# Kernel optimization log

Hardware: AMD Instinct MI355X
Metric: run time of the kernel (lower is better)

## Reference

```python
import jax, jax.numpy as jnp
import numpy as np

B, S, H, NH, DIS = 8, 512, 512, 8, 32
HD = H // NH  # head_dim = 64


def setup_inputs() -> dict:
    key = jax.random.key(0)
    ks = jax.random.split(key, 9)
    sc = 0.05
    return {
        "x": jax.random.normal(ks[0], (B, S, H), jnp.float32),
        "rel_distance": jax.random.randint(ks[1], (B, S, 2 * S), 0, DIS, jnp.int64),
        "mask": jnp.zeros((B, S, 2 * S), jnp.bool_),
        "query_pos_embedding": jax.random.normal(ks[2], (DIS, H), jnp.float32) * sc,
        "key_pos_embedding": jax.random.normal(ks[3], (DIS, H), jnp.float32) * sc,
        "value_pos_embedding": jax.random.normal(ks[4], (DIS, H), jnp.float32) * sc,
        "Wq": jax.random.normal(ks[5], (H, H), jnp.float32) * sc,
        "Wk": jax.random.normal(ks[6], (2 * H, H), jnp.float32) * sc,
        "Wv": jax.random.normal(ks[7], (2 * H, H), jnp.float32) * sc,
        "Wo": jax.random.normal(ks[8], (H, H), jnp.float32) * sc,
    }


def reference(x, rel_distance, mask, query_pos_embedding, key_pos_embedding,
              value_pos_embedding, Wq, Wk, Wv, Wo):
    b, s, _ = x.shape
    scale = jnp.sqrt(jnp.asarray(HD, x.dtype))

    # projections (torch Linear: y = x @ W.T)
    q = (x @ Wq.T).reshape(b, s, NH, HD).transpose(0, 2, 1, 3)        # [B,h,S,d]
    k = (x @ Wk.T).reshape(b, 2 * s, NH, HD).transpose(0, 2, 1, 3)    # [B,h,2S,d]
    v = (x @ Wv.T).reshape(b, 2 * s, NH, HD).transpose(0, 2, 1, 3)    # [B,h,2S,d]

    rel = jnp.broadcast_to(rel_distance[:, None], (b, NH, s, 2 * s))  # [B,h,S,2S]

    # relative-position weights via gather along distance axis
    q_emb = query_pos_embedding.reshape(DIS, NH, HD)                  # [n,h,d]
    qpw_full = jnp.einsum('bhsd,nhd->bhsn', q, q_emb)                 # [B,h,S,n]
    qpw = jnp.take_along_axis(qpw_full, rel, axis=3)                  # [B,h,S,2S]

    k_emb = key_pos_embedding.reshape(DIS, NH, HD)
    kpw_full = jnp.einsum('bhkd,nhd->bhkn', k, k_emb)                 # [B,h,2S,n]
    kpw = jnp.take_along_axis(kpw_full, rel.transpose(0, 1, 3, 2), axis=3)  # [B,h,2S,S]
    kpw = kpw.transpose(0, 1, 3, 2)                                   # [B,h,S,2S]

    scores = (jnp.einsum('bhsd,bhkd->bhsk', q, k) + qpw + kpw) / scale
    scores = jnp.where(mask[:, None], -jnp.inf, scores)
    probs = jax.nn.softmax(scores, axis=-1)                           # [B,h,S,2S]

    # scatter-add probs into distance buckets: [B,h,S,n]
    bi = jnp.arange(b)[:, None, None, None]
    hi = jnp.arange(NH)[None, :, None, None]
    si = jnp.arange(s)[None, None, :, None]
    vdw = jnp.zeros((b, NH, s, DIS), probs.dtype).at[bi, hi, si, rel].add(probs)

    v_emb = value_pos_embedding.reshape(DIS, NH, HD)                  # [n,h,d]
    out = jnp.einsum('bhsk,bhkd->bhsd', probs, v) \
        + jnp.einsum('bhsn,nhd->bhsd', vdw, v_emb)                    # [B,h,S,d]
    out = out.transpose(0, 2, 1, 3).reshape(b, s, H)
    return out @ Wo.T
```

## Files before the change

kernel.cpp:

```cpp
#include <hip/hip_runtime.h>
#include <math.h>

#define Bc 8
#define Sc 512
#define Hc 512
#define NHc 8
#define HDc 64
#define DISc 32
#define S2c 1024

typedef __attribute__((ext_vector_type(8))) short bf16x8;
typedef __attribute__((ext_vector_type(4))) float f32x4;
#define MFMA16(a, b, c) __builtin_amdgcn_mfma_f32_16x16x32_bf16(a, b, c, 0, 0, 0)

__device__ __forceinline__ unsigned short f2bf(float f) {
  unsigned u = __float_as_uint(f);
  return (unsigned short)((u + 0x7fffu + ((u >> 16) & 1u)) >> 16);
}
__device__ __forceinline__ float b2f(unsigned short u) {
  return __uint_as_float((unsigned)u << 16);
}
__device__ __forceinline__ bf16x8 ldb16x8(const unsigned short* p) {
  union { uint4 u; bf16x8 s; } cv;
  cv.u = *(const uint4*)p;
  return cv.s;
}
__device__ __forceinline__ void gll16(const unsigned short* g, void* l) {
  __builtin_amdgcn_global_load_lds(
      (const __attribute__((address_space(1))) unsigned int*)g,
      (__attribute__((address_space(3))) unsigned int*)l, 16, 0, 0);
}

__global__ __launch_bounds__(256) void cvt5_k(
    const float* __restrict__ x, const float* __restrict__ wq,
    const float* __restrict__ wk, const float* __restrict__ wv,
    const float* __restrict__ wo, unsigned short* __restrict__ x16,
    unsigned short* __restrict__ w16q, unsigned short* __restrict__ w16k,
    unsigned short* __restrict__ w16v, unsigned short* __restrict__ w16o) {
  int i = blockIdx.x * 256 + threadIdx.x;
  const float* src; unsigned short* dst; int off; float sc = 1.f;
  if (i < 524288)      { src = x;  dst = x16;  off = i; }
  else if (i < 589824) { src = wq; dst = w16q; off = i - 524288; sc = 0.125f; }
  else if (i < 720896) { src = wk; dst = w16k; off = i - 589824; }
  else if (i < 851968) { src = wv; dst = w16v; off = i - 720896; }
  else                 { src = wo; dst = w16o; off = i - 851968; }
  float4 v = ((const float4*)src)[off];
  ushort4 u;
  u.x = f2bf(v.x * sc); u.y = f2bf(v.y * sc);
  u.z = f2bf(v.z * sc); u.w = f2bf(v.w * sc);
  ((ushort4*)dst)[off] = u;
}

__global__ __launch_bounds__(256) void pack_k(const int* __restrict__ rel,
                                              const unsigned char* __restrict__ mask,
                                              unsigned char* __restrict__ pk8) {
  int i = blockIdx.x * 256 + threadIdx.x;
  const int* rp = rel + i * 16;
  uint4 mu = *(const uint4*)(mask + i * 16);
  const unsigned char* mb = (const unsigned char*)&mu;
  uint4 o;
  unsigned* ow = (unsigned*)&o;
#pragma unroll
  for (int g = 0; g < 4; ++g) {
    int4 r4 = ((const int4*)rp)[g];
    unsigned b0 = ((unsigned)r4.x & 31u) | (mb[g * 4 + 0] ? 0x80u : 0u);
    unsigned b1 = ((unsigned)r4.y & 31u) | (mb[g * 4 + 1] ? 0x80u : 0u);
    unsigned b2 = ((unsigned)r4.z & 31u) | (mb[g * 4 + 2] ? 0x80u : 0u);
    unsigned b3 = ((unsigned)r4.w & 31u) | (mb[g * 4 + 3] ? 0x80u : 0u);
    ow[g] = b0 | (b1 << 8) | (b2 << 16) | (b3 << 24);
  }
  *(uint4*)(pk8 + i * 16) = o;
}

__global__ __launch_bounds__(256) void wemb_k(
    const float* __restrict__ qpe, const float* __restrict__ kpe,
    const float* __restrict__ Wq, const float* __restrict__ Wk,
    unsigned short* __restrict__ wqp, unsigned short* __restrict__ wkp) {
  const int bid = blockIdx.x;
  const int cc = bid & 3, unit = bid >> 2;
  const int c0 = cc << 7;
  const int t = threadIdx.x;
  const float* emb; const float* Wsrc; unsigned short* outp; int rowbase, h;
  if (unit < 8) {
    h = unit; emb = qpe; Wsrc = Wq + (size_t)(h * 64) * 512; outp = wqp; rowbase = h * 32;
  } else {
    int u = unit - 8; int e = u >> 3; h = u & 7;
    emb = kpe; Wsrc = Wk + (size_t)(e * 512 + h * 64) * 512; outp = wkp;
    rowbase = e * 256 + h * 32;
  }
  __shared__ float es[32][65];
  __shared__ float wsh[64][132];
  {
    int n = t >> 3, d4 = (t & 7) << 3;
    float4 v0 = *(const float4*)(emb + (size_t)n * 512 + h * 64 + d4);
    float4 v1 = *(const float4*)(emb + (size_t)n * 512 + h * 64 + d4 + 4);
    *(float4*)&es[n][d4] = v0;
    *(float4*)&es[n][d4 + 4] = v1;
  }
#pragma unroll
  for (int p = 0; p < 8; ++p) {
    int slot = t + (p << 8);
    int d = slot >> 5, c4 = (slot & 31) << 2;
    *(float4*)&wsh[d][c4] = *(const float4*)(Wsrc + (size_t)d * 512 + c0 + c4);
  }
  __syncthreads();
  const int n = t >> 3, cb = (t & 7) << 4;
  float acc[16] = {};
#pragma unroll
  for (int d = 0; d < 64; ++d) {
    float ev = es[n][d];
    float4 w0 = *(const float4*)&wsh[d][cb];
    float4 w1 = *(const float4*)&wsh[d][cb + 4];
    float4 w2 = *(const float4*)&wsh[d][cb + 8];
    float4 w3 = *(const float4*)&wsh[d][cb + 12];
    acc[0] = fmaf(ev, w0.x, acc[0]);   acc[1] = fmaf(ev, w0.y, acc[1]);
    acc[2] = fmaf(ev, w0.z, acc[2]);   acc[3] = fmaf(ev, w0.w, acc[3]);
    acc[4] = fmaf(ev, w1.x, acc[4]);   acc[5] = fmaf(ev, w1.y, acc[5]);
    acc[6] = fmaf(ev, w1.z, acc[6]);   acc[7] = fmaf(ev, w1.w, acc[7]);
    acc[8] = fmaf(ev, w2.x, acc[8]);   acc[9] = fmaf(ev, w2.y, acc[9]);
    acc[10] = fmaf(ev, w2.z, acc[10]); acc[11] = fmaf(ev, w2.w, acc[11]);
    acc[12] = fmaf(ev, w3.x, acc[12]); acc[13] = fmaf(ev, w3.y, acc[13]);
    acc[14] = fmaf(ev, w3.z, acc[14]); acc[15] = fmaf(ev, w3.w, acc[15]);
  }
  unsigned short* orow = outp + (size_t)(rowbase + n) * 512 + c0 + cb;
#pragma unroll
  for (int j = 0; j < 16; ++j) orow[j] = f2bf(acc[j] * 0.125f);
}

template <int MODE>
__global__ __launch_bounds__(256, 4) void gemm16_k(
    const unsigned short* __restrict__ A, const unsigned short* __restrict__ B1,
    const unsigned short* __restrict__ B2, void* __restrict__ out1,
    void* __restrict__ out2, int M, int N, int K, int nsplit) {
  const int t = threadIdx.x;
  const int w = t >> 6, lane = t & 63, ln = lane & 15, qd = lane >> 4;
  const int wm = (w >> 1) << 6, wn = (w & 1) << 5;
  const int m0 = blockIdx.y << 7, n0 = blockIdx.x << 6;
  __shared__ __align__(16) unsigned short As[128 * 64];
  __shared__ __align__(16) unsigned short Bs[64 * 64];
  const bool reg1 = (n0 < nsplit);
  const unsigned short* Bb =
      reg1 ? B1 + (size_t)n0 * K : B2 + (size_t)(n0 - nsplit) * K;
  const int lr = lane >> 3, lc = (lane & 7) << 3;
  const unsigned short* ga = A + (size_t)(m0 + (w << 5) + lr) * K + lc;
  const unsigned short* gb = Bb + (size_t)((w << 4) + lr) * K + lc;
  char* lA = (char*)As + (w << 12);
  char* lB = (char*)Bs + (w << 11);
  f32x4 z = {0.f, 0.f, 0.f, 0.f};
  f32x4 acc[4][2] = {{z, z}, {z, z}, {z, z}, {z, z}};
  for (int k0 = 0; k0 < K; k0 += 64) {
#pragma unroll
    for (int i = 0; i < 4; ++i)
      gll16(ga + (size_t)(i << 3) * K + k0, lA + (i << 10));
#pragma unroll
    for (int i = 0; i < 2; ++i)
      gll16(gb + (size_t)(i << 3) * K + k0, lB + (i << 10));
    __syncthreads();
#pragma unroll
    for (int kk = 0; kk < 64; kk += 32) {
      bf16x8 af[4], bfr[2];
#pragma unroll
      for (int x = 0; x < 4; ++x)
        af[x] = ldb16x8(&As[(wm + x * 16 + ln) * 64 + kk + qd * 8]);
#pragma unroll
      for (int y = 0; y < 2; ++y)
        bfr[y] = ldb16x8(&Bs[(wn + y * 16 + ln) * 64 + kk + qd * 8]);
#pragma unroll
      for (int tm = 0; tm < 4; ++tm)
#pragma unroll
        for (int tn = 0; tn < 2; ++tn)
          acc[tm][tn] = MFMA16(af[tm], bfr[tn], acc[tm][tn]);
    }
    __syncthreads();
  }
#pragma unroll
  for (int tm = 0; tm < 4; ++tm)
#pragma unroll
    for (int tn = 0; tn < 2; ++tn)
#pragma unroll
      for (int r = 0; r < 4; ++r) {
        int m = m0 + wm + tm * 16 + qd * 4 + r;
        int n = n0 + wn + tn * 16 + ln;
        float v = acc[tm][tn][r];
        int bb = m >> 9, s = m & 511;
        if (MODE == 0) {
          ((float*)out1)[(size_t)m * N + n] = v;
        } else if (MODE == 3) {
          int e = n >> 9, hh = (n >> 6) & 7, d = n & 63;
          int k2 = 2 * s + e;
          ((unsigned short*)out1)[((size_t)(bb * 8 + hh) * 64 + d) * 1024 + k2] = f2bf(v);
        } else if (MODE == 1) {
          if (reg1) {
            int hh = (n >> 6) & 7, d = n & 63;
            ((unsigned short*)out1)[((size_t)(bb * 8 + hh) * 512 + s) * 64 + d] = f2bf(v);
          } else {
            int n2 = n - 512, hh = n2 >> 5, nn = n2 & 31;
            ((unsigned short*)out2)[((size_t)(bb * 8 + hh) * 512 + s) * 32 + nn] = f2bf(v);
          }
        } else {
          if (reg1) {
            int e = n >> 9, hh = (n >> 6) & 7, d = n & 63;
            int k2 = 2 * s + e;
            ((unsigned short*)out1)[((size_t)(bb * 8 + hh) * 1024 + k2) * 64 + d] = f2bf(v);
          } else {
            int n2 = n - 1024, e = n2 >> 8, hh = (n2 >> 5) & 7, nn = n2 & 31;
            int k2 = 2 * s + e;
            ((unsigned short*)out2)[((size_t)(bb * 8 + hh) * 1024 + k2) * 32 + nn] = f2bf(v);
          }
        }
      }
}

__global__ __launch_bounds__(512, 4) void attn6_k(
    const unsigned short* __restrict__ q16h, const unsigned short* __restrict__ kb16,
    const unsigned short* __restrict__ vT16, const unsigned short* __restrict__ qpw16,
    const unsigned short* __restrict__ kpw16, const unsigned char* __restrict__ pk8,
    const float* __restrict__ v_emb, unsigned short* __restrict__ attn16) {
  const int bid = blockIdx.x;
  const int b = bid & 7;
  const int h = (bid >> 3) & 7;
  const int qb = ((bid >> 6) & 7) << 6;
  const int t = threadIdx.x;
  const int w = t >> 6;
  const int g = w >> 2;
  const int ws4 = w & 3;
  const int lane = t & 63;
  const int ln = lane & 15;
  const int qd = lane >> 4;

  __shared__ __align__(16) char smem[60928];
  unsigned char*  pkt  = (unsigned char*)smem;
  unsigned short* kpws = (unsigned short*)(smem + 10240);
  unsigned short* q32s = (unsigned short*)(smem + 19456);
  unsigned short* pbuf = (unsigned short*)(smem + 24064);
  unsigned long long* vdwm64 = (unsigned long long*)(smem + 42496);
  float*          accbuf = (float*)smem;
  unsigned short* vest   = (unsigned short*)(smem + 24064);
  unsigned short* vdwb   = (unsigned short*)(smem + 29184);

  for (int i = t; i < 4 * 16 * 36; i += 512) vdwm64[i] = 0ull;
  if (t < 256) {
    int row = t >> 2, c8 = (t & 3) << 3;
    *(uint4*)&q32s[row * 36 + c8] =
        *(const uint4*)(qpw16 + ((size_t)((b * 8 + h) * 512 + qb) + row) * 32 + c8);
  }
  const unsigned short* kbase = kb16 + (size_t)(b * 8 + h) * 65536;
  const unsigned short* vbase = vT16 + (size_t)(b * 8 + h) * 65536;
  bf16x8 aQ[2];
  {
    const unsigned short* qsrc =
        q16h + ((size_t)((b * 8 + h) * 512 + qb + ws4 * 16 + ln)) * 64;
    aQ[0] = ldb16x8(qsrc + qd * 8);
    aQ[1] = ldb16x8(qsrc + 32 + qd * 8);
  }
  f32x4 z = {0.f, 0.f, 0.f, 0.f};
  f32x4 acc[4] = {z, z, z, z};

  const int u = t & 255, gg = t >> 8;
  const int qr = u >> 2, cg = (u & 3) << 4;
  const int kc8 = (u & 3) << 3;
  const unsigned char* pks = pk8 + ((size_t)(b * 512 + qb + qr)) * 1024 + (gg << 9);
  const unsigned short* kps =
      kpw16 + ((size_t)((b * 8 + h) * 1024) + (gg << 9) + qr) * 32 + kc8;
  unsigned char* pt_w = pkt + gg * 5120 + qr * 80 + cg;
  unsigned short* kp_w = kpws + gg * 2304 + qr * 36 + kc8;

  uint4 pv = *(const uint4*)(pks + cg);
  uint4 kv = *(const uint4*)kps;

  for (int kti = 0; kti < 8; ++kti) {
    *(uint4*)pt_w = pv;
    *(uint4*)kp_w = kv;
    __syncthreads();
    if (kti < 7) {
      pv = *(const uint4*)(pks + ((kti + 1) << 6) + cg);
      kv = *(const uint4*)(kps + ((size_t)(kti + 1) << 11));
    }
    const int kt0 = (kti + g * 8) << 6;

    f32x4 sc4[4];
#pragma unroll
    for (int t4 = 0; t4 < 4; ++t4) {
      f32x4 c = z;
      c = MFMA16(aQ[0], ldb16x8(kbase + (size_t)(kt0 + t4 * 16 + ln) * 64 + qd * 8), c);
      c = MFMA16(aQ[1], ldb16x8(kbase + (size_t)(kt0 + t4 * 16 + ln) * 64 + 32 + qd * 8), c);
      sc4[t4] = c;
    }

    unsigned char* pt_ = pkt + g * 5120;
    unsigned short* kp_ = kpws + g * 2304;
#pragma unroll
    for (int r = 0; r < 4; ++r) {
#pragma unroll
      for (int t4 = 0; t4 < 4; ++t4) {
        int row_l = ws4 * 16 + qd * 4 + r;
        int kl = t4 * 16 + ln;
        unsigned um = pt_[row_l * 80 + kl];
        int rd = um & 31;
        float s = sc4[t4][r] + b2f(q32s[row_l * 36 + rd]) + b2f(kp_[kl * 36 + rd]);
        float p = (um & 0x80u) ? 0.f : __expf(s);
        atomicAdd(&vdwm64[ws4 * 576 + (qd * 4 + r) * 36 + rd],
                  (unsigned long long)(p * 67108864.0f));
        pbuf[w * 1152 + (qd * 4 + r) * 72 + kl] = f2bf(p);
      }
    }

    bf16x8 a0 = ldb16x8(&pbuf[w * 1152 + ln * 72 + qd * 8]);
    bf16x8 a1 = ldb16x8(&pbuf[w * 1152 + ln * 72 + 32 + qd * 8]);
#pragma unroll
    for (int dt = 0; dt < 4; ++dt) {
      acc[dt] = MFMA16(a0, ldb16x8(vbase + (size_t)(dt * 16 + ln) * 1024 + kt0 + qd * 8), acc[dt]);
      acc[dt] = MFMA16(a1, ldb16x8(vbase + (size_t)(dt * 16 + ln) * 1024 + kt0 + 32 + qd * 8), acc[dt]);
    }
    __syncthreads();
  }

  if (t < 256) {
    int n = t >> 3, d0 = (t & 7) << 3;
    const float* src = v_emb + ((size_t)n << 9) + (h << 6) + d0;
    float4 f0 = *(const float4*)src;
    float4 f1 = *(const float4*)(src + 4);
    vest[(d0 + 0) * 40 + n] = f2bf(f0.x); vest[(d0 + 1) * 40 + n] = f2bf(f0.y);
    vest[(d0 + 2) * 40 + n] = f2bf(f0.z); vest[(d0 + 3) * 40 + n] = f2bf(f0.w);
    vest[(d0 + 4) * 40 + n] = f2bf(f1.x); vest[(d0 + 5) * 40 + n] = f2bf(f1.y);
    vest[(d0 + 6) * 40 + n] = f2bf(f1.z); vest[(d0 + 7) * 40 + n] = f2bf(f1.w);
  } else {
    int row = lane >> 2, n0 = (lane & 3) << 3;
    float vv[8];
#pragma unroll
    for (int j = 0; j < 8; ++j)
      vv[j] = (float)vdwm64[ws4 * 576 + row * 36 + n0 + j] * 1.4901161193847656e-8f;
    ushort4 u0, u1;
    u0.x = f2bf(vv[0]); u0.y = f2bf(vv[1]); u0.z = f2bf(vv[2]); u0.w = f2bf(vv[3]);
    u1.x = f2bf(vv[4]); u1.y = f2bf(vv[5]); u1.z = f2bf(vv[6]); u1.w = f2bf(vv[7]);
    *(ushort4*)&vdwb[ws4 * 640 + row * 40 + n0] = u0;
    *(ushort4*)&vdwb[ws4 * 640 + row * 40 + n0 + 4] = u1;
  }
  __syncthreads();

  if (g == 1) {
    bf16x8 av = ldb16x8(&vdwb[ws4 * 640 + ln * 40 + qd * 8]);
#pragma unroll
    for (int dt = 0; dt < 4; ++dt)
      acc[dt] = MFMA16(av, ldb16x8(&vest[(dt * 16 + ln) * 40 + qd * 8]), acc[dt]);
#pragma unroll
    for (int r = 0; r < 4; ++r)
#pragma unroll
      for (int dt = 0; dt < 4; ++dt)
        accbuf[ws4 * 1088 + (qd * 4 + r) * 68 + dt * 16 + ln] = acc[dt][r];
  }
  __syncthreads();

  if (g == 0) {
    float inv[4];
#pragma unroll
    for (int r = 0; r < 4; ++r) {
      unsigned long long lu = 0ull;
#pragma unroll
      for (int n = 0; n < 32; ++n)
        lu += vdwm64[ws4 * 576 + (qd * 4 + r) * 36 + n];
      inv[r] = 67108864.0f / (float)lu;
    }
    unsigned short* obase =
        attn16 + ((size_t)(b * 512 + qb + ws4 * 16 + qd * 4)) * 512 + (h << 6);
#pragma unroll
    for (int r = 0; r < 4; ++r)
#pragma unroll
      for (int dt = 0; dt < 4; ++dt) {
        float v = (acc[dt][r] + accbuf[ws4 * 1088 + (qd * 4 + r) * 68 + dt * 16 + ln]) * inv[r];
        obase[(size_t)r * 512 + dt * 16 + ln] = f2bf(v);
      }
  }
}

extern "C" void kernel_launch(void* const* d_in, const int* in_sizes, int n_in,
                              void* d_out, int out_size, void* d_ws, size_t ws_size,
                              hipStream_t stream) {
  const float* x = (const float*)d_in[0];
  const int* rel = (const int*)d_in[1];
  const unsigned char* mask = (const unsigned char*)d_in[2];
  const float* qpe = (const float*)d_in[3];
  const float* kpe = (const float*)d_in[4];
  const float* vpe = (const float*)d_in[5];
  const float* Wq = (const float*)d_in[6];
  const float* Wk = (const float*)d_in[7];
  const float* Wv = (const float*)d_in[8];
  const float* Wo = (const float*)d_in[9];
  float* out = (float*)d_out;

  unsigned short* u = (unsigned short*)d_ws;
  unsigned short* x16    = u;
  unsigned short* w16q   = x16 + 2097152;
  unsigned short* w16k   = w16q + 262144;
  unsigned short* w16v   = w16k + 524288;
  unsigned short* w16o   = w16v + 524288;
  unsigned short* wqp16  = w16o + 262144;
  unsigned short* wkp16  = wqp16 + 131072;
  unsigned short* q16h   = wkp16 + 262144;
  unsigned short* qpw16  = q16h + 2097152;
  unsigned short* kb16   = qpw16 + 1048576;
  unsigned short* kpw16  = kb16 + 4194304;
  unsigned short* vT16   = kpw16 + 2097152;
  unsigned short* attn16 = vT16 + 4194304;
  unsigned char* pk8 = (unsigned char*)(attn16 + 2097152);

  pack_k<<<1024, 256, 0, stream>>>(rel, mask, pk8);
  cvt5_k<<<3584, 256, 0, stream>>>(x, Wq, Wk, Wv, Wo, x16, w16q, w16k, w16v, w16o);
  wemb_k<<<96, 256, 0, stream>>>(qpe, kpe, Wq, Wk, wqp16, wkp16);
  gemm16_k<1><<<dim3(12, 32), 256, 0, stream>>>(x16, w16q, wqp16, q16h, qpw16,
                                                4096, 768, 512, 512);
  gemm16_k<2><<<dim3(24, 32), 256, 0, stream>>>(x16, w16k, wkp16, kb16, kpw16,
                                                4096, 1536, 512, 1024);
  gemm16_k<3><<<dim3(16, 32), 256, 0, stream>>>(x16, w16v, nullptr, vT16, nullptr,
                                                4096, 1024, 512, 1024);
  attn6_k<<<512, 512, 0, stream>>>(q16h, kb16, vT16, qpw16, kpw16, pk8, vpe, attn16);
  gemm16_k<0><<<dim3(8, 32), 256, 0, stream>>>(attn16, w16o, nullptr, out, nullptr,
                                               4096, 512, 512, 512);
}
```

Baseline: 231.0 us.

## Merge Q/K/V projection GEMMs into one launch and double-buffer LDS tiles

```diff
diff --git a/kernel.cpp b/kernel.cpp
--- a/kernel.cpp
+++ b/kernel.cpp
@@ -127,51 +127,63 @@
   for (int j = 0; j < 16; ++j) orow[j] = f2bf(acc[j] * 0.125f);
 }
 
-template <int MODE>
-__global__ __launch_bounds__(256, 4) void gemm16_k(
-    const unsigned short* __restrict__ A, const unsigned short* __restrict__ B1,
-    const unsigned short* __restrict__ B2, void* __restrict__ out1,
-    void* __restrict__ out2, int M, int N, int K, int nsplit) {
+__global__ __launch_bounds__(256, 3) void gemmqkv_k(
+    const unsigned short* __restrict__ A,
+    const unsigned short* __restrict__ wq, const unsigned short* __restrict__ wqp,
+    const unsigned short* __restrict__ wk, const unsigned short* __restrict__ wkp,
+    const unsigned short* __restrict__ wv,
+    unsigned short* __restrict__ q16h, unsigned short* __restrict__ qpw16,
+    unsigned short* __restrict__ kb16, unsigned short* __restrict__ kpw16,
+    unsigned short* __restrict__ vT16) {
   const int t = threadIdx.x;
   const int w = t >> 6, lane = t & 63, ln = lane & 15, qd = lane >> 4;
   const int wm = (w >> 1) << 6, wn = (w & 1) << 5;
   const int m0 = blockIdx.y << 7, n0 = blockIdx.x << 6;
-  __shared__ __align__(16) unsigned short As[128 * 64];
-  __shared__ __align__(16) unsigned short Bs[64 * 64];
-  const bool reg1 = (n0 < nsplit);
-  const unsigned short* Bb =
-      reg1 ? B1 + (size_t)n0 * K : B2 + (size_t)(n0 - nsplit) * K;
+  __shared__ __align__(16) unsigned short As[2][128 * 64];
+  __shared__ __align__(16) unsigned short Bs[2][64 * 64];
+  const unsigned short* Bb;
+  if (n0 < 512)        Bb = wq  + (size_t)n0 * 512;
+  else if (n0 < 768)   Bb = wqp + (size_t)(n0 - 512) * 512;
+  else if (n0 < 1792)  Bb = wk  + (size_t)(n0 - 768) * 512;
+  else if (n0 < 2304)  Bb = wkp + (size_t)(n0 - 1792) * 512;
+  else                 Bb = wv  + (size_t)(n0 - 2304) * 512;
   const int lr = lane >> 3, lc = (lane & 7) << 3;
-  const unsigned short* ga = A + (size_t)(m0 + (w << 5) + lr) * K + lc;
-  const unsigned short* gb = Bb + (size_t)((w << 4) + lr) * K + lc;
-  char* lA = (char*)As + (w << 12);
-  char* lB = (char*)Bs + (w << 11);
+  const unsigned short* ga = A + (size_t)(m0 + (w << 5) + lr) * 512 + lc;
+  const unsigned short* gb = Bb + (size_t)((w << 4) + lr) * 512 + lc;
   f32x4 z = {0.f, 0.f, 0.f, 0.f};
   f32x4 acc[4][2] = {{z, z}, {z, z}, {z, z}, {z, z}};
-  for (int k0 = 0; k0 < K; k0 += 64) {
-#pragma unroll
-    for (int i = 0; i < 4; ++i)
-      gll16(ga + (size_t)(i << 3) * K + k0, lA + (i << 10));
-#pragma unroll
-    for (int i = 0; i < 2; ++i)
-      gll16(gb + (size_t)(i << 3) * K + k0, lB + (i << 10));
+
+#define STAGE_QKV(buf, k0)                                             \
+  {                                                                    \
+    char* lA = (char*)&As[buf][0] + (w << 12);                         \
+    char* lB = (char*)&Bs[buf][0] + (w << 11);                         \
+    _Pragma("unroll") for (int i = 0; i < 4; ++i)                      \
+        gll16(ga + (size_t)(i << 3) * 512 + (k0), lA + (i << 10));     \
+    _Pragma("unroll") for (int i = 0; i < 2; ++i)                      \
+        gll16(gb + (size_t)(i << 3) * 512 + (k0), lB + (i << 10));     \
+  }
+
+  STAGE_QKV(0, 0);
+#pragma unroll
+  for (int ks = 0; ks < 8; ++ks) {
+    const int cur = ks & 1;
     __syncthreads();
+    if (ks < 7) STAGE_QKV(cur ^ 1, (ks + 1) << 6);
 #pragma unroll
     for (int kk = 0; kk < 64; kk += 32) {
       bf16x8 af[4], bfr[2];
 #pragma unroll
       for (int x = 0; x < 4; ++x)
-        af[x] = ldb16x8(&As[(wm + x * 16 + ln) * 64 + kk + qd * 8]);
+        af[x] = ldb16x8(&As[cur][(wm + x * 16 + ln) * 64 + kk + qd * 8]);
 #pragma unroll
       for (int y = 0; y < 2; ++y)
-        bfr[y] = ldb16x8(&Bs[(wn + y * 16 + ln) * 64 + kk + qd * 8]);
+        bfr[y] = ldb16x8(&Bs[cur][(wn + y * 16 + ln) * 64 + kk + qd * 8]);
 #pragma unroll
       for (int tm = 0; tm < 4; ++tm)
 #pragma unroll
         for (int tn = 0; tn < 2; ++tn)
           acc[tm][tn] = MFMA16(af[tm], bfr[tn], acc[tm][tn]);
     }
-    __syncthreads();
   }
 #pragma unroll
   for (int tm = 0; tm < 4; ++tm)
@@ -181,34 +193,90 @@
       for (int r = 0; r < 4; ++r) {
         int m = m0 + wm + tm * 16 + qd * 4 + r;
         int n = n0 + wn + tn * 16 + ln;
-        float v = acc[tm][tn][r];
+        unsigned short v16 = f2bf(acc[tm][tn][r]);
         int bb = m >> 9, s = m & 511;
-        if (MODE == 0) {
-          ((float*)out1)[(size_t)m * N + n] = v;
-        } else if (MODE == 3) {
-          int e = n >> 9, hh = (n >> 6) & 7, d = n & 63;
+        if (n0 < 512) {
+          int hh = (n >> 6) & 7, d = n & 63;
+          q16h[((size_t)(bb * 8 + hh) * 512 + s) * 64 + d] = v16;
+        } else if (n0 < 768) {
+          int n2 = n - 512, hh = n2 >> 5, nn = n2 & 31;
+          qpw16[((size_t)(bb * 8 + hh) * 512 + s) * 32 + nn] = v16;
+        } else if (n0 < 1792) {
+          int n2 = n - 768, e = n2 >> 9, hh = (n2 >> 6) & 7, d = n2 & 63;
           int k2 = 2 * s + e;
-          ((unsigned short*)out1)[((size_t)(bb * 8 + hh) * 64 + d) * 1024 + k2] = f2bf(v);
-        } else if (MODE == 1) {
-          if (reg1) {
-            int hh = (n >> 6) & 7, d = n & 63;
-            ((unsigned short*)out1)[((size_t)(bb * 8 + hh) * 512 + s) * 64 + d] = f2bf(v);
-          } else {
-            int n2 = n - 512, hh = n2 >> 5, nn = n2 & 31;
-            ((unsigned short*)out2)[((size_t)(bb * 8 + hh) * 512 + s) * 32 + nn] = f2bf(v);
-          }
+          kb16[((size_t)(bb * 8 + hh) * 1024 + k2) * 64 + d] = v16;
+        } else if (n0 < 2304) {
+          int n2 = n - 1792, e = n2 >> 8, hh = (n2 >> 5) & 7, nn = n2 & 31;
+          int k2 = 2 * s + e;
+          kpw16[((size_t)(bb * 8 + hh) * 1024 + k2) * 32 + nn] = v16;
         } else {
-          if (reg1) {
-            int e = n >> 9, hh = (n >> 6) & 7, d = n & 63;
-            int k2 = 2 * s + e;
-            ((unsigned short*)out1)[((size_t)(bb * 8 + hh) * 1024 + k2) * 64 + d] = f2bf(v);
-          } else {
-            int n2 = n - 1024, e = n2 >> 8, hh = (n2 >> 5) & 7, nn = n2 & 31;
-            int k2 = 2 * s + e;
-            ((unsigned short*)out2)[((size_t)(bb * 8 + hh) * 1024 + k2) * 32 + nn] = f2bf(v);
-          }
+          int n2 = n - 2304, e = n2 >> 9, hh = (n2 >> 6) & 7, d = n2 & 63;
+          int k2 = 2 * s + e;
+          vT16[((size_t)(bb * 8 + hh) * 64 + d) * 1024 + k2] = v16;
         }
       }
+#undef STAGE_QKV
+}
+
+__global__ __launch_bounds__(256, 3) void gemmo_k(
+    const unsigned short* __restrict__ A, const unsigned short* __restrict__ Bw,
+    float* __restrict__ out) {
+  const int t = threadIdx.x;
+  const int w = t >> 6, lane = t & 63, ln = lane & 15, qd = lane >> 4;
+  const int wm = (w >> 1) << 6, wn = (w & 1) << 5;
+  const int m0 = blockIdx.y << 7, n0 = blockIdx.x << 6;
+  __shared__ __align__(16) unsigned short As[2][128 * 64];
+  __shared__ __align__(16) unsigned short Bs[2][64 * 64];
+  const unsigned short* Bb = Bw + (size_t)n0 * 512;
+  const int lr = lane >> 3, lc = (lane & 7) << 3;
+  const unsigned short* ga = A + (size_t)(m0 + (w << 5) + lr) * 512 + lc;
+  const unsigned short* gb = Bb + (size_t)((w << 4) + lr) * 512 + lc;
+  f32x4 z = {0.f, 0.f, 0.f, 0.f};
+  f32x4 acc[4][2] = {{z, z}, {z, z}, {z, z}, {z, z}};
+
+#define STAGE_O(buf, k0)                                               \
+  {                                                                    \
+    char* lA = (char*)&As[buf][0] + (w << 12);                         \
+    char* lB = (char*)&Bs[buf][0] + (w << 11);                         \
+    _Pragma("unroll") for (int i = 0; i < 4; ++i)                      \
+        gll16(ga + (size_t)(i << 3) * 512 + (k0), lA + (i << 10));     \
+    _Pragma("unroll") for (int i = 0; i < 2; ++i)                      \
+        gll16(gb + (size_t)(i << 3) * 512 + (k0), lB + (i << 10));     \
+  }
+
+  STAGE_O(0, 0);
+#pragma unroll
+  for (int ks = 0; ks < 8; ++ks) {
+    const int cur = ks & 1;
+    __syncthreads();
+    if (ks < 7) STAGE_O(cur ^ 1, (ks + 1) << 6);
+#pragma unroll
+    for (int kk = 0; kk < 64; kk += 32) {
+      bf16x8 af[4], bfr[2];
+#pragma unroll
+      for (int x = 0; x < 4; ++x)
+        af[x] = ldb16x8(&As[cur][(wm + x * 16 + ln) * 64 + kk + qd * 8]);
+#pragma unroll
+      for (int y = 0; y < 2; ++y)
+        bfr[y] = ldb16x8(&Bs[cur][(wn + y * 16 + ln) * 64 + kk + qd * 8]);
+#pragma unroll
+      for (int tm = 0; tm < 4; ++tm)
+#pragma unroll
+        for (int tn = 0; tn < 2; ++tn)
+          acc[tm][tn] = MFMA16(af[tm], bfr[tn], acc[tm][tn]);
+    }
+  }
+#pragma unroll
+  for (int tm = 0; tm < 4; ++tm)
+#pragma unroll
+    for (int tn = 0; tn < 2; ++tn)
+#pragma unroll
+      for (int r = 0; r < 4; ++r) {
+        int m = m0 + wm + tm * 16 + qd * 4 + r;
+        int n = n0 + wn + tn * 16 + ln;
+        out[(size_t)m * 512 + n] = acc[tm][tn][r];
+      }
+#undef STAGE_O
 }
 
 __global__ __launch_bounds__(512, 4) void attn6_k(
@@ -407,13 +475,8 @@
   pack_k<<<1024, 256, 0, stream>>>(rel, mask, pk8);
   cvt5_k<<<3584, 256, 0, stream>>>(x, Wq, Wk, Wv, Wo, x16, w16q, w16k, w16v, w16o);
   wemb_k<<<96, 256, 0, stream>>>(qpe, kpe, Wq, Wk, wqp16, wkp16);
-  gemm16_k<1><<<dim3(12, 32), 256, 0, stream>>>(x16, w16q, wqp16, q16h, qpw16,
-                                                4096, 768, 512, 512);
-  gemm16_k<2><<<dim3(24, 32), 256, 0, stream>>>(x16, w16k, wkp16, kb16, kpw16,
-                                                4096, 1536, 512, 1024);
-  gemm16_k<3><<<dim3(16, 32), 256, 0, stream>>>(x16, w16v, nullptr, vT16, nullptr,
-                                                4096, 1024, 512, 1024);
+  gemmqkv_k<<<dim3(52, 32), 256, 0, stream>>>(x16, w16q, wqp16, w16k, wkp16, w16v,
+                                              q16h, qpw16, kb16, kpw16, vT16);
   attn6_k<<<512, 512, 0, stream>>>(q16h, kb16, vT16, qpw16, kpw16, pk8, vpe, attn16);
-  gemm16_k<0><<<dim3(8, 32), 256, 0, stream>>>(attn16, w16o, nullptr, out, nullptr,
-                                               4096, 512, 512, 512);
-}
+  gemmo_k<<<dim3(8, 32), 256, 0, stream>>>(attn16, w16o, out);
+}
```

After: 229.2 us. About the same (-0.8%).
